# Kernel tuning notes

Hardware: AMD Instinct MI355X
Metric: run time of the kernel (lower is better)

## Reference

```python
import jax, jax.numpy as jnp
import numpy as np

G, C_PER, C_IN, J, B, H, W, K = 8, 32, 256, 64, 16, 56, 56, 3


def setup_inputs() -> dict:
    key = jax.random.key(0)
    kx, kw, kb = jax.random.split(key, 3)
    x = jax.random.normal(kx, (B, C_IN, H, W), dtype=jnp.float32)
    # Per-cluster conv weights [G, j_rank, c, K, K] and biases [G, j_rank]
    weight = jax.random.normal(kw, (G, J, C_PER, K, K), dtype=jnp.float32) * 0.05
    bias = jax.random.normal(kb, (G, J), dtype=jnp.float32) * 0.01
    # Arrangements: 8 clusters of 32 non-contiguous channel indices (fixed permutation)
    arrangements = jnp.asarray(
        np.random.RandomState(0).permutation(C_IN).reshape(G, C_PER), dtype=jnp.int32
    )
    return {"x": x, "weight": weight, "bias": bias, "arrangements": arrangements}


def reference(x, weight, bias, arrangements):
    # Gather channel subsets: x[:, arr] -> [B, G, c, H, W] -> [G, B, c, H, W]
    xg = jnp.transpose(x[:, arrangements], (1, 0, 2, 3, 4))

    def conv1(xi, wi):
        # xi: [B, c, H, W], wi: [J, c, K, K]; stride 1, pad 1, dilation 1 (torch default cross-correlation)
        return jax.lax.conv_general_dilated(
            xi, wi,
            window_strides=(1, 1),
            padding=((1, 1), (1, 1)),
            dimension_numbers=("NCHW", "OIHW", "NCHW"),
        )

    out = jax.vmap(conv1)(xg, weight)              # [G, B, J, H, W]
    out = out + bias[:, None, :, None, None]
    g, b, j, h, w = out.shape
    # torch.cat(dim=1) over clusters -> [B, G*J, H, W]
    return jnp.transpose(out, (1, 0, 2, 3, 4)).reshape(b, g * j, h, w)
```

## Files before the change

### kernel.cpp

```cpp
#include <hip/hip_runtime.h>


#define NG 8
#define CPER 32
#define CIN 256
#define NJ 64
#define NB 16
#define NH 56
#define NW 56
#define PXSTRIDE 40
#define XS_SHORTS (6 * 58 * PXSTRIDE)
#define XSW_ELEMS (16 * 6 * 58)

typedef __attribute__((ext_vector_type(8))) short short8v;
typedef __attribute__((ext_vector_type(4))) float float4v;

__device__ __forceinline__ unsigned bf16rne(float f) {
    unsigned u = __float_as_uint(f);
    return (u + 0x7FFFu + ((u >> 16) & 1u)) >> 16;
}

__global__ __launch_bounds__(256, 4)
void gconv_mfma(const float* __restrict__ x,
                const float* __restrict__ w,
                const float* __restrict__ bias,
                const int* __restrict__ arr,
                float* __restrict__ out) {
    __shared__ __align__(16) unsigned short xs[XS_SHORTS];

    const int tid  = threadIdx.x;
    const int band = blockIdx.x;
    const int b    = blockIdx.y;
    const int g    = blockIdx.z;
    const int r0   = band * 4;
    const int lane = tid & 63;
    const int jt   = tid >> 6;
    const int n    = lane & 15;
    const int kq   = lane >> 4;

    for (int e = tid; e < XSW_ELEMS; e += 256) {
        int c2   = e / 348;
        int rem  = e - c2 * 348;
        int row  = rem / 58;
        int colp = rem - row * 58;
        int grow = r0 - 1 + row;
        int gcol = colp - 1;
        unsigned pack = 0;
        if ((unsigned)grow < (unsigned)NH && (unsigned)gcol < (unsigned)NW) {
            int ch0 = arr[g * CPER + c2 * 2];
            int ch1 = arr[g * CPER + c2 * 2 + 1];
            float v0 = x[((b * CIN + ch0) * NH + grow) * NW + gcol];
            float v1 = x[((b * CIN + ch1) * NH + grow) * NW + gcol];
            pack = bf16rne(v0) | (bf16rne(v1) << 16);
        }
        *(unsigned*)(&xs[(row * 58 + colp) * PXSTRIDE + c2 * 2]) = pack;
    }

    short8v A[9];
    {
        const float* wp = w + ((size_t)((g * NJ + jt * 16 + n) * CPER) + kq * 8) * 9;
        #pragma unroll
        for (int t = 0; t < 9; ++t) {
            short8v a;
            #pragma unroll
            for (int cc = 0; cc < 8; ++cc)
                a[cc] = (short)(unsigned short)bf16rne(wp[cc * 9 + t]);
            A[t] = a;
        }
    }
    float4v binit;
    #pragma unroll
    for (int i = 0; i < 4; ++i) binit[i] = bias[g * NJ + jt * 16 + kq * 4 + i];

    __syncthreads();

    int rl = 0, col = n;
    for (int t = 0; t < 14; ++t) {
        float4v acc = binit;
        const unsigned short* pb = xs + (rl * 58 + col) * PXSTRIDE + kq * 8;
        #pragma unroll
        for (int kh = 0; kh < 3; ++kh) {
            #pragma unroll
            for (int kw = 0; kw < 3; ++kw) {
                short8v bv = *(const short8v*)(pb + (kh * 58 + kw) * PXSTRIDE);
                acc = __builtin_amdgcn_mfma_f32_16x16x32_bf16(
                    A[kh * 3 + kw], bv, acc, 0, 0, 0);
            }
        }
        int ob = (((b * (NG * NJ) + g * NJ + jt * 16 + kq * 4) * NH
                   + (r0 + rl)) * NW) + col;
        #pragma unroll
        for (int i = 0; i < 4; ++i)
            out[ob + i * (NH * NW)] = acc[i];

        col += 16;
        if (col >= NW) { col -= NW; rl += 1; }
    }
}

extern "C" void kernel_launch(void* const* d_in, const int* in_sizes, int n_in,
                              void* d_out, int out_size, void* d_ws, size_t ws_size,
                              hipStream_t stream) {
    const float* x    = (const float*)d_in[0];
    const float* wght = (const float*)d_in[1];
    const float* bias = (const float*)d_in[2];
    const int*   arr  = (const int*)d_in[3];
    float* out = (float*)d_out;

    dim3 grid(14, NB, NG);
    gconv_mfma<<<grid, 256, 0, stream>>>(x, wght, bias, arr, out);
}
```

Measured before the change: 202.3 us.

## Double-buffer row bands in LDS with register prefetch and staged weights

Each block now walks 14 output rows in 2-row bands instead of computing one 4-row band. The next band's global loads are prefetched into registers while MFMAs run on the current LDS buffer, and the result is written to the alternate buffer. Weights are converted once through LDS with vector loads instead of strided scalar global loads. Gather addresses are precomputed per thread, and two MFMA accumulation chains are interleaved for ILP. The grid shrinks to 512 blocks and launch bounds drop to 2 blocks per SIMD, which cuts parallelism and raises register pressure.

```diff
diff --git a/kernel.cpp b/kernel.cpp
--- a/kernel.cpp
+++ b/kernel.cpp
@@ -8,9 +8,11 @@
 #define NB 16
 #define NH 56
 #define NW 56
-#define PXSTRIDE 40
-#define XS_SHORTS (6 * 58 * PXSTRIDE)
-#define XSW_ELEMS (16 * 6 * 58)
+#define PXST 40
+#define BUFSH (4 * 58 * PXST)
+#define NPACK (16 * 4 * 58)
+#define NITER 15
+#define WEI_SH (9 * 2048)
 
 typedef __attribute__((ext_vector_type(8))) short short8v;
 typedef __attribute__((ext_vector_type(4))) float float4v;
@@ -20,81 +22,144 @@
     return (u + 0x7FFFu + ((u >> 16) & 1u)) >> 16;
 }
 
-__global__ __launch_bounds__(256, 4)
+__global__ __launch_bounds__(256, 2)
 void gconv_mfma(const float* __restrict__ x,
                 const float* __restrict__ w,
                 const float* __restrict__ bias,
                 const int* __restrict__ arr,
                 float* __restrict__ out) {
-    __shared__ __align__(16) unsigned short xs[XS_SHORTS];
+    __shared__ __align__(16) unsigned short smem[2 * BUFSH];
 
-    const int tid  = threadIdx.x;
-    const int band = blockIdx.x;
-    const int b    = blockIdx.y;
-    const int g    = blockIdx.z;
-    const int r0   = band * 4;
-    const int lane = tid & 63;
-    const int jt   = tid >> 6;
-    const int n    = lane & 15;
-    const int kq   = lane >> 4;
+    const int tid   = threadIdx.x;
+    const int chunk = blockIdx.x;
+    const int b     = blockIdx.y;
+    const int g     = blockIdx.z;
+    const int lane  = tid & 63;
+    const int jt    = tid >> 6;
+    const int n     = lane & 15;
+    const int kq    = lane >> 4;
 
-    for (int e = tid; e < XSW_ELEMS; e += 256) {
-        int c2   = e / 348;
-        int rem  = e - c2 * 348;
-        int row  = rem / 58;
-        int colp = rem - row * 58;
-        int grow = r0 - 1 + row;
-        int gcol = colp - 1;
-        unsigned pack = 0;
-        if ((unsigned)grow < (unsigned)NH && (unsigned)gcol < (unsigned)NW) {
-            int ch0 = arr[g * CPER + c2 * 2];
-            int ch1 = arr[g * CPER + c2 * 2 + 1];
-            float v0 = x[((b * CIN + ch0) * NH + grow) * NW + gcol];
-            float v1 = x[((b * CIN + ch1) * NH + grow) * NW + gcol];
-            pack = bf16rne(v0) | (bf16rne(v1) << 16);
+    {
+        const float* wg = w + (size_t)g * (NJ * CPER * 9);
+        for (int e = tid; e < WEI_SH; e += 256) {
+            int jc = e / 9, tap = e - jc * 9;
+            smem[tap * 2048 + jc] = (unsigned short)bf16rne(wg[e]);
         }
-        *(unsigned*)(&xs[(row * 58 + colp) * PXSTRIDE + c2 * 2]) = pack;
     }
-
+    __syncthreads();
     short8v A[9];
     {
-        const float* wp = w + ((size_t)((g * NJ + jt * 16 + n) * CPER) + kq * 8) * 9;
+        const unsigned short* wl = smem + (jt * 16 + n) * CPER + kq * 8;
         #pragma unroll
-        for (int t = 0; t < 9; ++t) {
-            short8v a;
-            #pragma unroll
-            for (int cc = 0; cc < 8; ++cc)
-                a[cc] = (short)(unsigned short)bf16rne(wp[cc * 9 + t]);
-            A[t] = a;
-        }
+        for (int t = 0; t < 9; ++t) A[t] = *(const short8v*)(wl + t * 2048);
     }
     float4v binit;
     #pragma unroll
     for (int i = 0; i < 4; ++i) binit[i] = bias[g * NJ + jt * 16 + kq * 4 + i];
-
     __syncthreads();
 
-    int rl = 0, col = n;
-    for (int t = 0; t < 14; ++t) {
-        float4v acc = binit;
-        const unsigned short* pb = xs + (rl * 58 + col) * PXSTRIDE + kq * 8;
+    int pre0[NITER], pre1[NITER], meta[NITER];
+    #pragma unroll
+    for (int k = 0; k < NITER; ++k) {
+        int e = tid + 256 * k;
+        int act = e < NPACK;
+        int c2 = e / 232;
+        int rem = e - c2 * 232;
+        int row = rem / 58;
+        int colp = rem - row * 58;
+        int ch0 = 0, ch1 = 0;
+        if (act) { ch0 = arr[g * CPER + c2 * 2]; ch1 = arr[g * CPER + c2 * 2 + 1]; }
+        pre0[k] = ch0 * (NH * NW) + (row - 1) * NW + (colp - 1);
+        pre1[k] = ch1 * (NH * NW) + (row - 1) * NW + (colp - 1);
+        int cv = act && ((unsigned)(colp - 1) < NW);
+        meta[k] = ((row * 58 + colp) * PXST + c2 * 2) | (row << 14) | (cv << 16) | (act << 17);
+    }
+    const float* xb = x + (size_t)b * (CIN * NH * NW);
+
+    float f0[NITER], f1[NITER];
+    int r0 = chunk * 14;
+
+    {
+        int roff = r0 * NW;
         #pragma unroll
-        for (int kh = 0; kh < 3; ++kh) {
+        for (int k = 0; k < NITER; ++k) {
+            int row = (meta[k] >> 14) & 3;
+            int v = ((meta[k] >> 16) & 1) && ((unsigned)(r0 + row - 1) < NH);
+            f0[k] = v ? xb[pre0[k] + roff] : 0.0f;
+            f1[k] = v ? xb[pre1[k] + roff] : 0.0f;
+        }
+        #pragma unroll
+        for (int k = 0; k < NITER; ++k) {
+            if ((meta[k] >> 17) & 1)
+                *(unsigned*)(&smem[meta[k] & 0x3FFF]) =
+                    bf16rne(f0[k]) | (bf16rne(f1[k]) << 16);
+        }
+    }
+    __syncthreads();
+
+    for (int bd = 0; bd < 7; ++bd) {
+        if (bd < 6) {
+            int r1 = r0 + 2, roff = r1 * NW;
             #pragma unroll
-            for (int kw = 0; kw < 3; ++kw) {
-                short8v bv = *(const short8v*)(pb + (kh * 58 + kw) * PXSTRIDE);
-                acc = __builtin_amdgcn_mfma_f32_16x16x32_bf16(
-                    A[kh * 3 + kw], bv, acc, 0, 0, 0);
+            for (int k = 0; k < NITER; ++k) {
+                int row = (meta[k] >> 14) & 3;
+                int v = ((meta[k] >> 16) & 1) && ((unsigned)(r1 + row - 1) < NH);
+                f0[k] = v ? xb[pre0[k] + roff] : 0.0f;
+                f1[k] = v ? xb[pre1[k] + roff] : 0.0f;
             }
         }
-        int ob = (((b * (NG * NJ) + g * NJ + jt * 16 + kq * 4) * NH
-                   + (r0 + rl)) * NW) + col;
-        #pragma unroll
-        for (int i = 0; i < 4; ++i)
-            out[ob + i * (NH * NW)] = acc[i];
-
-        col += 16;
-        if (col >= NW) { col -= NW; rl += 1; }
+        {
+            const unsigned short* buf = smem + (bd & 1) * BUFSH;
+            const int obase = ((b * (NG * NJ) + g * NJ + jt * 16 + kq * 4) * NH + r0) * NW;
+            int rl = 0, col = n;
+            #pragma unroll
+            for (int tp = 0; tp < 3; ++tp) {
+                int rlA = rl, colA = col; col += 16; if (col >= NW) { col -= NW; ++rl; }
+                int rlB = rl, colB = col; col += 16; if (col >= NW) { col -= NW; ++rl; }
+                const unsigned short* pA = buf + (rlA * 58 + colA) * PXST + kq * 8;
+                const unsigned short* pB = buf + (rlB * 58 + colB) * PXST + kq * 8;
+                float4v a0 = binit, a1 = binit;
+                #pragma unroll
+                for (int kh = 0; kh < 3; ++kh)
+                    #pragma unroll
+                    for (int kw = 0; kw < 3; ++kw) {
+                        short8v b0 = *(const short8v*)(pA + (kh * 58 + kw) * PXST);
+                        short8v b1 = *(const short8v*)(pB + (kh * 58 + kw) * PXST);
+                        a0 = __builtin_amdgcn_mfma_f32_16x16x32_bf16(A[kh * 3 + kw], b0, a0, 0, 0, 0);
+                        a1 = __builtin_amdgcn_mfma_f32_16x16x32_bf16(A[kh * 3 + kw], b1, a1, 0, 0, 0);
+                    }
+                int obA = obase + rlA * NW + colA;
+                int obB = obase + rlB * NW + colB;
+                #pragma unroll
+                for (int i = 0; i < 4; ++i) {
+                    out[obA + i * (NH * NW)] = a0[i];
+                    out[obB + i * (NH * NW)] = a1[i];
+                }
+            }
+            const unsigned short* pA = buf + (rl * 58 + col) * PXST + kq * 8;
+            float4v a0 = binit;
+            #pragma unroll
+            for (int kh = 0; kh < 3; ++kh)
+                #pragma unroll
+                for (int kw = 0; kw < 3; ++kw) {
+                    short8v b0 = *(const short8v*)(pA + (kh * 58 + kw) * PXST);
+                    a0 = __builtin_amdgcn_mfma_f32_16x16x32_bf16(A[kh * 3 + kw], b0, a0, 0, 0, 0);
+                }
+            int obA = obase + rl * NW + col;
+            #pragma unroll
+            for (int i = 0; i < 4; ++i) out[obA + i * (NH * NW)] = a0[i];
+        }
+        if (bd < 6) {
+            unsigned short* dst = smem + ((bd + 1) & 1) * BUFSH;
+            #pragma unroll
+            for (int k = 0; k < NITER; ++k) {
+                if ((meta[k] >> 17) & 1)
+                    *(unsigned*)(&dst[meta[k] & 0x3FFF]) =
+                        bf16rne(f0[k]) | (bf16rne(f1[k]) << 16);
+            }
+            r0 += 2;
+            __syncthreads();
+        }
     }
 }
 
@@ -107,6 +172,6 @@
     const int*   arr  = (const int*)d_in[3];
     float* out = (float*)d_out;
 
-    dim3 grid(14, NB, NG);
+    dim3 grid(4, NB, NG);
     gconv_mfma<<<grid, 256, 0, stream>>>(x, wght, bias, arr, out);
 }
```

Result: faster. 184.5 us (-8.8%).
